# Optimization experiments

Hardware: AMD Instinct MI355X
Metric: run time of the kernel (lower is better)

Reference implementation:

```python
import math
import jax, jax.numpy as jnp
import numpy as np

DIM = 1024
NUM_HEADS = 16
HEAD_DIM = DIM // NUM_HEADS
SCALE = HEAD_DIM ** -0.5
ROPE_BASE = 10000.0


def _rope(x):
    # x: [b, h, t, d]; rotate-half RoPE as in the torch module
    b, h, t, d = x.shape
    half = d // 2
    freqs = jnp.exp(-math.log(ROPE_BASE) * jnp.arange(half, dtype=jnp.float32) / half)
    pos = jnp.arange(t, dtype=jnp.float32)
    angles = pos[:, None] * freqs[None, :]          # [t, half]
    sin = jnp.sin(angles)[None, None, :, :]
    cos = jnp.cos(angles)[None, None, :, :]
    x1, x2 = x[..., :half], x[..., half:]
    return jnp.concatenate([x1 * cos - x2 * sin, x1 * sin + x2 * cos], axis=-1)


def setup_inputs() -> dict:
    key = jax.random.key(0)
    k1, k2, k3, k4 = jax.random.split(key, 4)
    b, t = 2, 2048
    x = jax.random.normal(k1, (b, t, DIM), dtype=jnp.float32)
    # nn.Linear(dim, 3*dim, bias=False): store as [in, out] for x @ W
    w_qkv = jax.random.normal(k2, (DIM, 3 * DIM), dtype=jnp.float32) * (DIM ** -0.5)
    w_proj = jax.random.normal(k3, (DIM, DIM), dtype=jnp.float32) * (DIM ** -0.5)
    b_proj = jax.random.normal(k4, (DIM,), dtype=jnp.float32) * 0.02
    return {"x": x, "w_qkv": w_qkv, "w_proj": w_proj, "b_proj": b_proj}


def reference(x, w_qkv, w_proj, b_proj):
    b, t, c = x.shape
    h, hd = NUM_HEADS, HEAD_DIM
    qkv = (x @ w_qkv).reshape(b, t, 3, h, hd)
    qkv = jnp.transpose(qkv, (2, 0, 3, 1, 4))      # [3, b, h, t, hd]
    q, k, v = qkv[0], qkv[1], qkv[2]
    q, k = _rope(q), _rope(k)
    attn = jnp.einsum('bhqd,bhkd->bhqk', q, k) * SCALE
    causal_mask = jnp.triu(jnp.ones((t, t), dtype=bool), k=1)
    attn = jnp.where(causal_mask[None, None], -jnp.inf, attn)
    attn = jax.nn.softmax(attn, axis=-1)
    out = jnp.einsum('bhqk,bhkd->bhqd', attn, v)
    out = jnp.transpose(out, (0, 2, 1, 3)).reshape(b, t, c)
    return out @ w_proj + b_proj
```

## Files before the change

### kernel.cpp

```cpp
#include <hip/hip_runtime.h>
#include <math.h>

typedef unsigned short u16;
typedef unsigned int u32;
typedef __bf16 bfrag8 __attribute__((ext_vector_type(8)));
typedef float f32x4 __attribute__((ext_vector_type(4)));

#define B_ 2
#define T_ 2048
#define H_ 16
#define D_ 64
#define C_ 1024
#define NQKV_ 3072

#define MFMA_BF16(a, b, c) __builtin_amdgcn_mfma_f32_16x16x32_bf16((a), (b), (c), 0, 0, 0)

__device__ __forceinline__ u16 f2bf(float f) {
  u32 u = __builtin_bit_cast(u32, f);
  u += 0x7fffu + ((u >> 16) & 1u);
  return (u16)(u >> 16);
}

__device__ __forceinline__ void load_lds16(const u16* gp, u16* lp) {
  __builtin_amdgcn_global_load_lds(
      (const __attribute__((address_space(1))) u32*)(const void*)gp,
      (__attribute__((address_space(3))) u32*)(void*)lp, 16, 0, 0);
}

__global__ __launch_bounds__(256) void convert_x(const float* __restrict__ src,
                                                 u16* __restrict__ dst) {
  size_t i = ((size_t)blockIdx.x * 256 + threadIdx.x) * 8;
  const float* s = src + i;
  float4 a = *(const float4*)s, b = *(const float4*)(s + 4);
  union { uint4 v; u16 h[8]; } t;
  t.h[0] = f2bf(a.x); t.h[1] = f2bf(a.y); t.h[2] = f2bf(a.z); t.h[3] = f2bf(a.w);
  t.h[4] = f2bf(b.x); t.h[5] = f2bf(b.y); t.h[6] = f2bf(b.z); t.h[7] = f2bf(b.w);
  *(uint4*)(dst + i) = t.v;
}

__global__ __launch_bounds__(256) void transpose_w(const float* __restrict__ src,
                                                   u16* __restrict__ dst, int K, int N) {
  __shared__ u16 tile[64][65];
  int bx = blockIdx.x * 64;
  int by = blockIdx.y * 64;
  for (int idx = threadIdx.x; idx < 4096; idx += 256) {
    int r = idx >> 6, c = idx & 63;
    tile[r][c] = f2bf(src[(size_t)(by + r) * N + bx + c]);
  }
  __syncthreads();
  for (int idx = threadIdx.x; idx < 4096; idx += 256) {
    int r = idx >> 6, c = idx & 63;
    dst[(size_t)(bx + r) * K + by + c] = tile[c][r];
  }
}

__global__ __launch_bounds__(256) void gemm_qkv_rope(const u16* __restrict__ X,
                                                     const u16* __restrict__ WT,
                                                     u16* __restrict__ qb,
                                                     u16* __restrict__ kb,
                                                     u16* __restrict__ vb) {
  const int K = C_;
  __shared__ __align__(16) u16 As[2][128 * 64];
  __shared__ __align__(16) u16 Bs[2][128 * 64];
  int tid = threadIdx.x;
  int lane = tid & 63, wave = tid >> 6;
  int quad = lane >> 4, lr = lane & 15;
  int m0 = blockIdx.y * 128, n0 = blockIdx.x * 128;
  int wrow = (wave >> 1) * 64, wcol = (wave & 1) * 64;
  int r0 = wave * 32;
  int srow = lane >> 3;
  int schunk = (lane & 7) ^ srow;

  int koff0 = ((quad ^ (lr & 7)) << 3);
  int koff1 = (((4 | quad) ^ (lr & 7)) << 3);

  f32x4 zero = {0.f, 0.f, 0.f, 0.f};
  f32x4 acc[4][4];
#pragma unroll
  for (int i = 0; i < 4; i++)
#pragma unroll
    for (int j = 0; j < 4; j++) acc[i][j] = zero;

  const u16* ga = X + (size_t)(m0 + r0 + srow) * K + schunk * 8;
  const u16* gb = WT + (size_t)(n0 + r0 + srow) * K + schunk * 8;

#pragma unroll
  for (int l = 0; l < 4; l++) {
    load_lds16(ga + (size_t)(l * 8) * K, &As[0][(r0 + l * 8) * 64]);
    load_lds16(gb + (size_t)(l * 8) * K, &Bs[0][(r0 + l * 8) * 64]);
  }

  int buf = 0;
  for (int k0 = 0; k0 < K; k0 += 64) {
    __syncthreads();
    if (k0 + 64 < K) {
#pragma unroll
      for (int l = 0; l < 4; l++) {
        load_lds16(ga + (size_t)(l * 8) * K + k0 + 64, &As[buf ^ 1][(r0 + l * 8) * 64]);
        load_lds16(gb + (size_t)(l * 8) * K + k0 + 64, &Bs[buf ^ 1][(r0 + l * 8) * 64]);
      }
    }
    bfrag8 af[4][2], bf[4][2];
#pragma unroll
    for (int i = 0; i < 4; i++) {
      const u16* ar = &As[buf][(wrow + i * 16 + lr) * 64];
      af[i][0] = *(const bfrag8*)(ar + koff0);
      af[i][1] = *(const bfrag8*)(ar + koff1);
    }
#pragma unroll
    for (int j = 0; j < 4; j++) {
      const u16* br = &Bs[buf][(wcol + j * 16 + lr) * 64];
      bf[j][0] = *(const bfrag8*)(br + koff0);
      bf[j][1] = *(const bfrag8*)(br + koff1);
    }
#pragma unroll
    for (int i = 0; i < 4; i++)
#pragma unroll
      for (int j = 0; j < 4; j++) {
        acc[i][j] = MFMA_BF16(af[i][0], bf[j][0], acc[i][j]);
        acc[i][j] = MFMA_BF16(af[i][1], bf[j][1], acc[i][j]);
      }
    buf ^= 1;
  }

  int colbase = n0 + wcol;
  int which = colbase >> 10;
  int h = (colbase & 1023) >> 6;
  u16* dst = which == 0 ? qb : (which == 1 ? kb : vb);
  float sc0 = (which == 0) ? 0.125f : 1.0f;
  float fr0 = __expf(-0.28782313662425574f * (float)lr);
  float fr1 = __expf(-0.28782313662425574f * (float)(16 + lr));
#pragma unroll
  for (int i = 0; i < 4; i++) {
#pragma unroll
    for (int r = 0; r < 4; r++) {
      int m = m0 + wrow + i * 16 + quad * 4 + r;
      int b = m >> 11, tt = m & 2047;
      size_t base = ((size_t)(b * H_ + h) * T_ + tt) * D_;
      if (which < 2) {
        float sn, cs;
        __sincosf((float)tt * fr0, &sn, &cs);
        dst[base + lr] = f2bf((acc[i][0][r] * cs - acc[i][2][r] * sn) * sc0);
        dst[base + lr + 32] = f2bf((acc[i][0][r] * sn + acc[i][2][r] * cs) * sc0);
        __sincosf((float)tt * fr1, &sn, &cs);
        dst[base + 16 + lr] = f2bf((acc[i][1][r] * cs - acc[i][3][r] * sn) * sc0);
        dst[base + 48 + lr] = f2bf((acc[i][1][r] * sn + acc[i][3][r] * cs) * sc0);
      } else {
#pragma unroll
        for (int j = 0; j < 4; j++) dst[base + j * 16 + lr] = f2bf(acc[i][j][r]);
      }
    }
  }
}

__global__ __launch_bounds__(256) void transpose_v(const u16* __restrict__ v,
                                                   u16* __restrict__ vt) {
  __shared__ u16 tile[64][72];
  int t0 = blockIdx.x * 64;
  int bh = blockIdx.y;
  const u16* src = v + (size_t)bh * T_ * D_;
  u16* dst = vt + (size_t)bh * D_ * T_;
  for (int idx = threadIdx.x; idx < 512; idx += 256) {
    int r = idx >> 3, c8 = (idx & 7) * 8;
    *(uint4*)&tile[r][c8] = *(const uint4*)(src + (size_t)(t0 + r) * D_ + c8);
  }
  __syncthreads();
  for (int idx = threadIdx.x; idx < 512; idx += 256) {
    int d = idx >> 3, t8 = (idx & 7) * 8;
    union { uint4 u; u16 s[8]; } p;
#pragma unroll
    for (int e = 0; e < 8; e++) p.s[e] = tile[t8 + e][d];
    *(uint4*)(dst + (size_t)d * T_ + t0 + t8) = p.u;
  }
}

__global__ __launch_bounds__(256) void attn_k(const u16* __restrict__ qb,
                                              const u16* __restrict__ kb,
                                              const u16* __restrict__ vtb,
                                              u16* __restrict__ ob) {
  __shared__ __align__(16) u16 Ks[2][64 * 64];
  __shared__ __align__(16) u16 Vt[2][64 * 64];
  __shared__ __align__(16) u16 Pst[4][16 * 72];
  int tid = threadIdx.x;
  int lane = tid & 63, wave = tid >> 6;
  int quad = lane >> 4, lr = lane & 15;
  int i = blockIdx.x;
  int bq = 31 - (i >> 5);
  int bh = i & 31;
  int b = bh >> 4, h = bh & 15;
  const u16* Q = qb + (size_t)bh * T_ * D_;
  const u16* Kp = kb + (size_t)bh * T_ * D_;
  const u16* Vp = vtb + (size_t)bh * D_ * T_;
  int qr0 = bq * 64 + wave * 16;
  int r0 = wave * 16;
  int sr = lane >> 3;
  int sc = (((lane & 7) ^ (sr & 7)) * 8);

  int koff0 = ((quad ^ (lr & 7)) << 3);
  int koff1 = (((4 | quad) ^ (lr & 7)) << 3);

  bfrag8 qf[2];
#pragma unroll
  for (int ks = 0; ks < 2; ks++)
    qf[ks] = *(const bfrag8*)(Q + (size_t)(qr0 + lr) * D_ + ks * 32 + quad * 8);

  f32x4 zero = {0.f, 0.f, 0.f, 0.f};
  f32x4 o[4];
#pragma unroll
  for (int nn = 0; nn < 4; nn++) o[nn] = zero;
  float psum = 0.f;

  const u16* gk = Kp + (size_t)(r0 + sr) * D_ + sc;
  const u16* gv = Vp + (size_t)(r0 + sr) * T_ + sc;
  int niter = bq + 1;

  load_lds16(gk, &Ks[0][r0 * 64]);
  load_lds16(gk + (size_t)8 * D_, &Ks[0][(r0 + 8) * 64]);
  load_lds16(gv, &Vt[0][r0 * 64]);
  load_lds16(gv + (size_t)8 * T_, &Vt[0][(r0 + 8) * 64]);

  int buf = 0;
  int qloc = wave * 16 + lr;
  for (int it = 0; it < niter; it++) {
    __syncthreads();
    if (it + 1 < niter) {
      int tkn = (it + 1) * 64;
      load_lds16(gk + (size_t)tkn * D_, &Ks[buf ^ 1][r0 * 64]);
      load_lds16(gk + (size_t)(tkn + 8) * D_, &Ks[buf ^ 1][(r0 + 8) * 64]);
      load_lds16(gv + tkn, &Vt[buf ^ 1][r0 * 64]);
      load_lds16(gv + (size_t)8 * T_ + tkn, &Vt[buf ^ 1][(r0 + 8) * 64]);
    }
    const u16* ks_ = Ks[buf];
    const u16* vt_ = Vt[buf];

    f32x4 s[4];
#pragma unroll
    for (int j = 0; j < 4; j++) s[j] = zero;
#pragma unroll
    for (int j = 0; j < 4; j++) {
      bfrag8 kf0 = *(const bfrag8*)&ks_[(j * 16 + lr) * 64 + koff0];
      bfrag8 kf1 = *(const bfrag8*)&ks_[(j * 16 + lr) * 64 + koff1];
      s[j] = MFMA_BF16(kf0, qf[0], s[j]);
      s[j] = MFMA_BF16(kf1, qf[1], s[j]);
    }

    bool edge = (it == bq);
#pragma unroll
    for (int j = 0; j < 4; j++) {
      float p[4];
#pragma unroll
      for (int r = 0; r < 4; r++) {
        float e = __expf(s[j][r]);
        if (edge) {
          int kvloc = j * 16 + quad * 4 + r;
          e = (kvloc <= qloc) ? e : 0.f;
        }
        p[r] = e;
        psum += e;
      }
      u32 u0 = __builtin_bit_cast(u32, p[0]) + 0x8000u;
      u32 u1 = __builtin_bit_cast(u32, p[1]) + 0x8000u;
      u32 u2 = __builtin_bit_cast(u32, p[2]) + 0x8000u;
      u32 u3 = __builtin_bit_cast(u32, p[3]) + 0x8000u;
      uint2 pk;
      pk.x = (u0 >> 16) | (u1 & 0xffff0000u);
      pk.y = (u2 >> 16) | (u3 & 0xffff0000u);
      *(uint2*)&Pst[wave][lr * 72 + j * 16 + quad * 4] = pk;
    }

#pragma unroll
    for (int ks = 0; ks < 2; ks++) {
      bfrag8 pf = *(const bfrag8*)&Pst[wave][lr * 72 + ks * 32 + quad * 8];
      int ko = ks ? koff1 : koff0;
#pragma unroll
      for (int nn = 0; nn < 4; nn++) {
        bfrag8 vf = *(const bfrag8*)&vt_[(nn * 16 + lr) * 64 + ko];
        o[nn] = MFMA_BF16(pf, vf, o[nn]);
      }
    }
    buf ^= 1;
  }

  float l = psum;
  l += __shfl_xor(l, 16, 64);
  l += __shfl_xor(l, 32, 64);
  float linv = 1.0f / l;

#pragma unroll
  for (int r = 0; r < 4; r++) {
    float lrec = __shfl(linv, quad * 4 + r, 64);
    int row = qr0 + quad * 4 + r;
#pragma unroll
    for (int nn = 0; nn < 4; nn++)
      ob[(size_t)(b * T_ + row) * C_ + h * 64 + nn * 16 + lr] = f2bf(o[nn][r] * lrec);
  }
}

__global__ __launch_bounds__(256) void gemm_proj(const u16* __restrict__ A,
                                                 const u16* __restrict__ WT,
                                                 const float* __restrict__ bias,
                                                 float* __restrict__ out) {
  const int K = C_;
  __shared__ __align__(16) u16 As[2][64 * 32];
  __shared__ __align__(16) u16 Bs[2][128 * 32];
  int tid = threadIdx.x;
  int lane = tid & 63, wave = tid >> 6;
  int quad = lane >> 4, lr = lane & 15;
  int m0 = blockIdx.y * 64, n0 = blockIdx.x * 128;
  int wcol = wave * 32;
  int srow = lane >> 2, skc = (lane & 3) * 8;

  f32x4 zero = {0.f, 0.f, 0.f, 0.f};
  f32x4 acc[4][2];
#pragma unroll
  for (int i = 0; i < 4; i++)
#pragma unroll
    for (int j = 0; j < 2; j++) acc[i][j] = zero;

  const u16* ga = A + (size_t)(m0 + wave * 16 + srow) * K + skc;
  const u16* gb0 = WT + (size_t)(n0 + wave * 32 + srow) * K + skc;
  const u16* gb1 = WT + (size_t)(n0 + wave * 32 + 16 + srow) * K + skc;

  load_lds16(ga, &As[0][wave * 16 * 32]);
  load_lds16(gb0, &Bs[0][wave * 32 * 32]);
  load_lds16(gb1, &Bs[0][(wave * 32 + 16) * 32]);

  int buf = 0;
  for (int k0 = 0; k0 < K; k0 += 32) {
    __syncthreads();
    if (k0 + 32 < K) {
      load_lds16(ga + k0 + 32, &As[buf ^ 1][wave * 16 * 32]);
      load_lds16(gb0 + k0 + 32, &Bs[buf ^ 1][wave * 32 * 32]);
      load_lds16(gb1 + k0 + 32, &Bs[buf ^ 1][(wave * 32 + 16) * 32]);
    }
    bfrag8 af[4], bfr[2];
#pragma unroll
    for (int i = 0; i < 4; i++)
      af[i] = *(const bfrag8*)&As[buf][(i * 16 + lr) * 32 + quad * 8];
#pragma unroll
    for (int j = 0; j < 2; j++)
      bfr[j] = *(const bfrag8*)&Bs[buf][(wcol + j * 16 + lr) * 32 + quad * 8];
#pragma unroll
    for (int i = 0; i < 4; i++)
#pragma unroll
      for (int j = 0; j < 2; j++) acc[i][j] = MFMA_BF16(af[i], bfr[j], acc[i][j]);
    buf ^= 1;
  }

#pragma unroll
  for (int i = 0; i < 4; i++)
#pragma unroll
    for (int r = 0; r < 4; r++) {
      int m = m0 + i * 16 + quad * 4 + r;
#pragma unroll
      for (int j = 0; j < 2; j++) {
        int n = n0 + wcol + j * 16 + lr;
        out[(size_t)m * C_ + n] = acc[i][j][r] + bias[n];
      }
    }
}

extern "C" void kernel_launch(void* const* d_in, const int* in_sizes, int n_in,
                              void* d_out, int out_size, void* d_ws, size_t ws_size,
                              hipStream_t stream) {
  const float* x = (const float*)d_in[0];
  const float* w_qkv = (const float*)d_in[1];
  const float* w_proj = (const float*)d_in[2];
  const float* b_proj = (const float*)d_in[3];

  char* w = (char*)d_ws;
  u16* xb = (u16*)(w + 256);
  u16* vtb = xb;
  u16* regA = xb + (size_t)4096 * 1024;
  u16* wqkvT = regA;
  u16* abuf = regA;
  u16* wprojT = regA + (size_t)4096 * 1024;
  u16* qbuf = wprojT + (size_t)1024 * 1024;
  u16* kbuf = qbuf + (size_t)B_ * H_ * T_ * D_;
  u16* vbuf = kbuf + (size_t)B_ * H_ * T_ * D_;

  convert_x<<<2048, 256, 0, stream>>>(x, xb);
  transpose_w<<<dim3(NQKV_ / 64, C_ / 64), 256, 0, stream>>>(w_qkv, wqkvT, C_, NQKV_);
  transpose_w<<<dim3(C_ / 64, C_ / 64), 256, 0, stream>>>(w_proj, wprojT, C_, C_);
  gemm_qkv_rope<<<dim3(NQKV_ / 128, (B_ * T_) / 128), 256, 0, stream>>>(xb, wqkvT, qbuf, kbuf, vbuf);
  transpose_v<<<dim3(T_ / 64, B_ * H_), 256, 0, stream>>>(vbuf, vtb);
  attn_k<<<1024, 256, 0, stream>>>(qbuf, kbuf, vtb, abuf);
  gemm_proj<<<dim3(C_ / 128, (B_ * T_) / 64), 256, 0, stream>>>(abuf, wprojT, b_proj, (float*)d_out);
}
```

Measured before the change: 193.9 us.

## Widen attention blocks to 128 queries and deepen proj GEMM K-tile with swizzle

The attention kernel now runs 512-thread blocks covering 128 query rows with 8 waves. All waves share each 64-key K/V tile loaded into LDS, and waves past the causal edge skip compute. This halves K/V global traffic per query and cuts the block count, at the cost of some idle waves on the diagonal tile. The projection GEMM moves from a 32-wide to a 64-wide K step with an XOR-swizzled LDS layout, halving barriers and loop iterations and reducing bank conflicts, but it uses more LDS.

```diff
diff --git a/kernel.cpp b/kernel.cpp
--- a/kernel.cpp
+++ b/kernel.cpp
@@ -174,27 +174,27 @@
   }
 }
 
-__global__ __launch_bounds__(256) void attn_k(const u16* __restrict__ qb,
+__global__ __launch_bounds__(512) void attn_k(const u16* __restrict__ qb,
                                               const u16* __restrict__ kb,
                                               const u16* __restrict__ vtb,
                                               u16* __restrict__ ob) {
   __shared__ __align__(16) u16 Ks[2][64 * 64];
   __shared__ __align__(16) u16 Vt[2][64 * 64];
-  __shared__ __align__(16) u16 Pst[4][16 * 72];
+  __shared__ __align__(16) u16 Pst[8][16 * 72];
   int tid = threadIdx.x;
   int lane = tid & 63, wave = tid >> 6;
   int quad = lane >> 4, lr = lane & 15;
   int i = blockIdx.x;
-  int bq = 31 - (i >> 5);
+  int bq = 15 - (i >> 5);
   int bh = i & 31;
   int b = bh >> 4, h = bh & 15;
   const u16* Q = qb + (size_t)bh * T_ * D_;
   const u16* Kp = kb + (size_t)bh * T_ * D_;
   const u16* Vp = vtb + (size_t)bh * D_ * T_;
-  int qr0 = bq * 64 + wave * 16;
-  int r0 = wave * 16;
+  int qr0 = bq * 128 + wave * 16;
+  int r0v = wave * 8;
   int sr = lane >> 3;
-  int sc = (((lane & 7) ^ (sr & 7)) * 8);
+  int sc = (((lane & 7) ^ sr) * 8);
 
   int koff0 = ((quad ^ (lr & 7)) << 3);
   int koff1 = (((4 | quad) ^ (lr & 7)) << 3);
@@ -210,72 +210,71 @@
   for (int nn = 0; nn < 4; nn++) o[nn] = zero;
   float psum = 0.f;
 
-  const u16* gk = Kp + (size_t)(r0 + sr) * D_ + sc;
-  const u16* gv = Vp + (size_t)(r0 + sr) * T_ + sc;
-  int niter = bq + 1;
-
-  load_lds16(gk, &Ks[0][r0 * 64]);
-  load_lds16(gk + (size_t)8 * D_, &Ks[0][(r0 + 8) * 64]);
-  load_lds16(gv, &Vt[0][r0 * 64]);
-  load_lds16(gv + (size_t)8 * T_, &Vt[0][(r0 + 8) * 64]);
+  const u16* gk = Kp + (size_t)(r0v + sr) * D_ + sc;
+  const u16* gv = Vp + (size_t)(r0v + sr) * T_ + sc;
+  int niter = 2 * bq + 2;
+  int wlast = 2 * bq + (wave >> 2);
+  int qloc = (wave & 3) * 16 + lr;
+
+  load_lds16(gk, &Ks[0][r0v * 64]);
+  load_lds16(gv, &Vt[0][r0v * 64]);
 
   int buf = 0;
-  int qloc = wave * 16 + lr;
   for (int it = 0; it < niter; it++) {
     __syncthreads();
     if (it + 1 < niter) {
       int tkn = (it + 1) * 64;
-      load_lds16(gk + (size_t)tkn * D_, &Ks[buf ^ 1][r0 * 64]);
-      load_lds16(gk + (size_t)(tkn + 8) * D_, &Ks[buf ^ 1][(r0 + 8) * 64]);
-      load_lds16(gv + tkn, &Vt[buf ^ 1][r0 * 64]);
-      load_lds16(gv + (size_t)8 * T_ + tkn, &Vt[buf ^ 1][(r0 + 8) * 64]);
-    }
-    const u16* ks_ = Ks[buf];
-    const u16* vt_ = Vt[buf];
-
-    f32x4 s[4];
-#pragma unroll
-    for (int j = 0; j < 4; j++) s[j] = zero;
-#pragma unroll
-    for (int j = 0; j < 4; j++) {
-      bfrag8 kf0 = *(const bfrag8*)&ks_[(j * 16 + lr) * 64 + koff0];
-      bfrag8 kf1 = *(const bfrag8*)&ks_[(j * 16 + lr) * 64 + koff1];
-      s[j] = MFMA_BF16(kf0, qf[0], s[j]);
-      s[j] = MFMA_BF16(kf1, qf[1], s[j]);
-    }
-
-    bool edge = (it == bq);
-#pragma unroll
-    for (int j = 0; j < 4; j++) {
-      float p[4];
-#pragma unroll
-      for (int r = 0; r < 4; r++) {
-        float e = __expf(s[j][r]);
-        if (edge) {
-          int kvloc = j * 16 + quad * 4 + r;
-          e = (kvloc <= qloc) ? e : 0.f;
+      load_lds16(gk + (size_t)tkn * D_, &Ks[buf ^ 1][r0v * 64]);
+      load_lds16(gv + tkn, &Vt[buf ^ 1][r0v * 64]);
+    }
+    if (it <= wlast) {
+      const u16* ks_ = Ks[buf];
+      const u16* vt_ = Vt[buf];
+
+      f32x4 s[4];
+#pragma unroll
+      for (int j = 0; j < 4; j++) s[j] = zero;
+#pragma unroll
+      for (int j = 0; j < 4; j++) {
+        bfrag8 kf0 = *(const bfrag8*)&ks_[(j * 16 + lr) * 64 + koff0];
+        bfrag8 kf1 = *(const bfrag8*)&ks_[(j * 16 + lr) * 64 + koff1];
+        s[j] = MFMA_BF16(kf0, qf[0], s[j]);
+        s[j] = MFMA_BF16(kf1, qf[1], s[j]);
+      }
+
+      bool edge = (it == wlast);
+#pragma unroll
+      for (int j = 0; j < 4; j++) {
+        float p[4];
+#pragma unroll
+        for (int r = 0; r < 4; r++) {
+          float e = __expf(s[j][r]);
+          if (edge) {
+            int kvloc = j * 16 + quad * 4 + r;
+            e = (kvloc <= qloc) ? e : 0.f;
+          }
+          p[r] = e;
+          psum += e;
         }
-        p[r] = e;
-        psum += e;
-      }
-      u32 u0 = __builtin_bit_cast(u32, p[0]) + 0x8000u;
-      u32 u1 = __builtin_bit_cast(u32, p[1]) + 0x8000u;
-      u32 u2 = __builtin_bit_cast(u32, p[2]) + 0x8000u;
-      u32 u3 = __builtin_bit_cast(u32, p[3]) + 0x8000u;
-      uint2 pk;
-      pk.x = (u0 >> 16) | (u1 & 0xffff0000u);
-      pk.y = (u2 >> 16) | (u3 & 0xffff0000u);
-      *(uint2*)&Pst[wave][lr * 72 + j * 16 + quad * 4] = pk;
-    }
-
-#pragma unroll
-    for (int ks = 0; ks < 2; ks++) {
-      bfrag8 pf = *(const bfrag8*)&Pst[wave][lr * 72 + ks * 32 + quad * 8];
-      int ko = ks ? koff1 : koff0;
-#pragma unroll
-      for (int nn = 0; nn < 4; nn++) {
-        bfrag8 vf = *(const bfrag8*)&vt_[(nn * 16 + lr) * 64 + ko];
-        o[nn] = MFMA_BF16(pf, vf, o[nn]);
+        u32 u0 = __builtin_bit_cast(u32, p[0]) + 0x8000u;
+        u32 u1 = __builtin_bit_cast(u32, p[1]) + 0x8000u;
+        u32 u2 = __builtin_bit_cast(u32, p[2]) + 0x8000u;
+        u32 u3 = __builtin_bit_cast(u32, p[3]) + 0x8000u;
+        uint2 pk;
+        pk.x = (u0 >> 16) | (u1 & 0xffff0000u);
+        pk.y = (u2 >> 16) | (u3 & 0xffff0000u);
+        *(uint2*)&Pst[wave][lr * 72 + j * 16 + quad * 4] = pk;
+      }
+
+#pragma unroll
+      for (int ks = 0; ks < 2; ks++) {
+        bfrag8 pf = *(const bfrag8*)&Pst[wave][lr * 72 + ks * 32 + quad * 8];
+        int ko = ks ? koff1 : koff0;
+#pragma unroll
+        for (int nn = 0; nn < 4; nn++) {
+          bfrag8 vf = *(const bfrag8*)&vt_[(nn * 16 + lr) * 64 + ko];
+          o[nn] = MFMA_BF16(pf, vf, o[nn]);
+        }
       }
     }
     buf ^= 1;
@@ -301,14 +300,18 @@
                                                  const float* __restrict__ bias,
                                                  float* __restrict__ out) {
   const int K = C_;
-  __shared__ __align__(16) u16 As[2][64 * 32];
-  __shared__ __align__(16) u16 Bs[2][128 * 32];
+  __shared__ __align__(16) u16 As[2][64 * 64];
+  __shared__ __align__(16) u16 Bs[2][128 * 64];
   int tid = threadIdx.x;
   int lane = tid & 63, wave = tid >> 6;
   int quad = lane >> 4, lr = lane & 15;
   int m0 = blockIdx.y * 64, n0 = blockIdx.x * 128;
   int wcol = wave * 32;
-  int srow = lane >> 2, skc = (lane & 3) * 8;
+  int srow = lane >> 3;
+  int schunk = (lane & 7) ^ srow;
+
+  int koff0 = ((quad ^ (lr & 7)) << 3);
+  int koff1 = (((4 | quad) ^ (lr & 7)) << 3);
 
   f32x4 zero = {0.f, 0.f, 0.f, 0.f};
   f32x4 acc[4][2];
@@ -317,33 +320,45 @@
 #pragma unroll
     for (int j = 0; j < 2; j++) acc[i][j] = zero;
 
-  const u16* ga = A + (size_t)(m0 + wave * 16 + srow) * K + skc;
-  const u16* gb0 = WT + (size_t)(n0 + wave * 32 + srow) * K + skc;
-  const u16* gb1 = WT + (size_t)(n0 + wave * 32 + 16 + srow) * K + skc;
-
-  load_lds16(ga, &As[0][wave * 16 * 32]);
-  load_lds16(gb0, &Bs[0][wave * 32 * 32]);
-  load_lds16(gb1, &Bs[0][(wave * 32 + 16) * 32]);
+  const u16* ga = A + (size_t)(m0 + wave * 16 + srow) * K + schunk * 8;
+  const u16* gb = WT + (size_t)(n0 + wave * 32 + srow) * K + schunk * 8;
+
+  load_lds16(ga, &As[0][(wave * 16) * 64]);
+  load_lds16(ga + (size_t)8 * K, &As[0][(wave * 16 + 8) * 64]);
+#pragma unroll
+  for (int l = 0; l < 4; l++)
+    load_lds16(gb + (size_t)(l * 8) * K, &Bs[0][(wave * 32 + l * 8) * 64]);
 
   int buf = 0;
-  for (int k0 = 0; k0 < K; k0 += 32) {
+  for (int k0 = 0; k0 < K; k0 += 64) {
     __syncthreads();
-    if (k0 + 32 < K) {
-      load_lds16(ga + k0 + 32, &As[buf ^ 1][wave * 16 * 32]);
-      load_lds16(gb0 + k0 + 32, &Bs[buf ^ 1][wave * 32 * 32]);
-      load_lds16(gb1 + k0 + 32, &Bs[buf ^ 1][(wave * 32 + 16) * 32]);
-    }
-    bfrag8 af[4], bfr[2];
+    if (k0 + 64 < K) {
+      load_lds16(ga + k0 + 64, &As[buf ^ 1][(wave * 16) * 64]);
+      load_lds16(ga + (size_t)8 * K + k0 + 64, &As[buf ^ 1][(wave * 16 + 8) * 64]);
+#pragma unroll
+      for (int l = 0; l < 4; l++)
+        load_lds16(gb + (size_t)(l * 8) * K + k0 + 64, &Bs[buf ^ 1][(wave * 32 + l * 8) * 64]);
+    }
+    bfrag8 af[4][2], bf[2][2];
+#pragma unroll
+    for (int i = 0; i < 4; i++) {
+      const u16* ar = &As[buf][(i * 16 + lr) * 64];
+      af[i][0] = *(const bfrag8*)(ar + koff0);
+      af[i][1] = *(const bfrag8*)(ar + koff1);
+    }
+#pragma unroll
+    for (int j = 0; j < 2; j++) {
+      const u16* br = &Bs[buf][(wcol + j * 16 + lr) * 64];
+      bf[j][0] = *(const bfrag8*)(br + koff0);
+      bf[j][1] = *(const bfrag8*)(br + koff1);
+    }
 #pragma unroll
     for (int i = 0; i < 4; i++)
-      af[i] = *(const bfrag8*)&As[buf][(i * 16 + lr) * 32 + quad * 8];
-#pragma unroll
-    for (int j = 0; j < 2; j++)
-      bfr[j] = *(const bfrag8*)&Bs[buf][(wcol + j * 16 + lr) * 32 + quad * 8];
-#pragma unroll
-    for (int i = 0; i < 4; i++)
-#pragma unroll
-      for (int j = 0; j < 2; j++) acc[i][j] = MFMA_BF16(af[i], bfr[j], acc[i][j]);
+#pragma unroll
+      for (int j = 0; j < 2; j++) {
+        acc[i][j] = MFMA_BF16(af[i][0], bf[j][0], acc[i][j]);
+        acc[i][j] = MFMA_BF16(af[i][1], bf[j][1], acc[i][j]);
+      }
     buf ^= 1;
   }
 
@@ -384,6 +399,6 @@
   transpose_w<<<dim3(C_ / 64, C_ / 64), 256, 0, stream>>>(w_proj, wprojT, C_, C_);
   gemm_qkv_rope<<<dim3(NQKV_ / 128, (B_ * T_) / 128), 256, 0, stream>>>(xb, wqkvT, qbuf, kbuf, vbuf);
   transpose_v<<<dim3(T_ / 64, B_ * H_), 256, 0, stream>>>(vbuf, vtb);
-  attn_k<<<1024, 256, 0, stream>>>(qbuf, kbuf, vtb, abuf);
+  attn_k<<<512, 512, 0, stream>>>(qbuf, kbuf, vtb, abuf);
   gemm_proj<<<dim3(C_ / 128, (B_ * T_) / 64), 256, 0, stream>>>(abuf, wprojT, b_proj, (float*)d_out);
 }
```

After: 196.9 us. Within noise of the previous version (+1.5%).
